# Kernel tuning notes

Hardware: AMD Instinct MI355X
Metric: run time of the kernel (lower is better)

Reference implementation:

```python
import jax, jax.numpy as jnp
import numpy as np

EPS = 1e-12  # torch F.normalize clamp epsilon
NOISE = np.array([1e-05, 2e-05, 3e-05], dtype=np.float32)  # diagonal regularizer


def setup_inputs() -> dict:
    key = jax.random.key(0)
    B, C = 65536, 128
    v_feat = jax.random.normal(key, (B, C, 3), dtype=jnp.float32)
    return {"v_feat": v_feat}


def reference(v_feat):
    # L2 normalize each 3-vector (B, C, 3) along last dim
    norm = jnp.sqrt(jnp.sum(v_feat * v_feat, axis=-1, keepdims=True))
    v = v_feat / jnp.maximum(norm, EPS)

    # Covariance M = v^T v  -> (B, 3, 3), plus tiny diagonal noise for stability
    M = jnp.einsum('bci,bcj->bij', v, v) + jnp.diag(jnp.asarray(NOISE))[None, :, :]

    # Batched symmetric 3x3 eigendecomposition (ascending eigenvalues)
    _, evecs = jnp.linalg.eigh(M)  # evecs: (B, 3, 3), columns are eigenvectors
    v1 = evecs[:, :, 0]  # (B, 3)
    v2 = evecs[:, :, 1]

    # Sign disambiguation: align with the mean direction of the features
    def fix_sign(vec):
        s = jnp.sign(jnp.sum(v * vec[:, None, :], axis=(1, 2)))  # (B,)
        s = jnp.where(s == 0, 1.0, s)
        return vec * s[:, None]

    v1 = fix_sign(v1)
    v2 = fix_sign(v2)
    v3 = jnp.cross(v1, v2)

    # Frame: columns [v1 v2 v3] -> (B, 3, 3)
    return jnp.stack([v1, v2, v3], axis=-1)
```

## Files before the change

kernel.cpp:

```cpp
#include <hip/hip_runtime.h>
#include <math.h>


#define WAVES_PER_BLOCK 4
#define BLOCK (WAVES_PER_BLOCK * 64)
#define ITERS 2
#define BATCHES_PER_WAVE (4 * ITERS)
#define BPB (WAVES_PER_BLOCK * BATCHES_PER_WAVE)

__device__ __forceinline__ double fast_rsqrt1(double x) {
    double r = (double)__builtin_amdgcn_rsqf((float)x);
    double h = -0.5 * x;
    r = r * fma(h, r * r, 1.5);
    return r;
}
__device__ __forceinline__ double fast_rsqrt2(double x) {
    double r = (double)__builtin_amdgcn_rsqf((float)x);
    double h = -0.5 * x;
    r = r * fma(h, r * r, 1.5);
    r = r * fma(h, r * r, 1.5);
    return r;
}
__device__ __forceinline__ double fast_rcp(double x) {
    double r = (double)__builtin_amdgcn_rcpf((float)x);
    r = r * fma(-x, r, 2.0);
    r = r * fma(-x, r, 2.0);
    return r;
}

template <int P, int Q, int R>
__device__ __forceinline__ void jrot(double (&A)[3][3], double (&V)[3][3]) {
    double apq = A[P][Q];
    if (fabs(apq) > 1e-18) {
        double theta = (A[Q][Q] - A[P][P]) * 0.5 * fast_rcp(apq);
        double q = fma(theta, theta, 1.0);
        double sq = (q < 1e37) ? q * fast_rsqrt2(q) : fabs(theta);
        double t = fast_rcp(fabs(theta) + sq);
        if (theta < 0.0) t = -t;
        double c = fast_rsqrt2(fma(t, t, 1.0));
        double s = t * c;
        double apq_t = t * apq;
        A[P][P] = A[P][P] - apq_t;
        A[Q][Q] = A[Q][Q] + apq_t;
        A[P][Q] = 0.0;
        A[Q][P] = 0.0;
        double apr = A[P][R], aqr = A[Q][R];
        A[P][R] = c * apr - s * aqr; A[R][P] = A[P][R];
        A[Q][R] = s * apr + c * aqr; A[R][Q] = A[Q][R];
#pragma unroll
        for (int i = 0; i < 3; ++i) {
            double vip = V[i][P], viq = V[i][Q];
            V[i][P] = c * vip - s * viq;
            V[i][Q] = s * vip + c * viq;
        }
    }
}

__global__ __launch_bounds__(BLOCK) void vn_frame_kernel(
    const float* __restrict__ vf, float* __restrict__ out, int B) {
    __shared__ double sM[BPB][9];

    const int tid  = threadIdx.x;
    const int wave = tid >> 6;
    const int lane = tid & 63;
    const int g    = lane >> 4;
    const int sub  = lane & 15;

    const int blockBase = blockIdx.x * BPB;

#pragma unroll
    for (int it = 0; it < ITERS; ++it) {
        const int bslot = wave * BATCHES_PER_WAVE + it * 4 + g;
        const int b = blockBase + bslot;
        if (b < B) {
            const float4* p4 =
                reinterpret_cast<const float4*>(vf + (size_t)b * 384 + sub * 24);
            float f[24];
#pragma unroll
            for (int i = 0; i < 6; ++i) {
                float4 q = p4[i];
                f[4 * i + 0] = q.x; f[4 * i + 1] = q.y;
                f[4 * i + 2] = q.z; f[4 * i + 3] = q.w;
            }

            double m[9];
#pragma unroll
            for (int k = 0; k < 9; ++k) m[k] = 0.0;

#pragma unroll
            for (int k = 0; k < 8; ++k) {
                float fx = f[3 * k + 0];
                float fy = f[3 * k + 1];
                float fz = f[3 * k + 2];
                float n2f = fmaf(fx, fx, fmaf(fy, fy, fz * fz));
                double n2 = (double)n2f;
                double inv = (n2 > 1e-24) ? fast_rsqrt1(n2) : 1e12;
                double x = (double)fx * inv;
                double y = (double)fy * inv;
                double z = (double)fz * inv;
                m[0] = fma(x, x, m[0]);
                m[1] = fma(x, y, m[1]);
                m[2] = fma(x, z, m[2]);
                m[3] = fma(y, y, m[3]);
                m[4] = fma(y, z, m[4]);
                m[5] = fma(z, z, m[5]);
                m[6] += x; m[7] += y; m[8] += z;
            }
#pragma unroll
            for (int off = 1; off < 16; off <<= 1) {
#pragma unroll
                for (int k = 0; k < 9; ++k) m[k] += __shfl_xor(m[k], off);
            }
            if (sub == 0) {
#pragma unroll
                for (int k = 0; k < 9; ++k) sM[bslot][k] = m[k];
            }
        }
    }

    __syncthreads();

    if (tid < BPB) {
        const int b = blockBase + tid;
        if (b < B) {
            double m[9];
#pragma unroll
            for (int k = 0; k < 9; ++k) m[k] = sM[tid][k];

            double A[3][3], V[3][3];
            A[0][0] = m[0] + (double)1e-05f;
            A[0][1] = m[1]; A[1][0] = m[1];
            A[0][2] = m[2]; A[2][0] = m[2];
            A[1][1] = m[3] + (double)2e-05f;
            A[1][2] = m[4]; A[2][1] = m[4];
            A[2][2] = m[5] + (double)3e-05f;
#pragma unroll
            for (int i = 0; i < 3; ++i)
#pragma unroll
                for (int j = 0; j < 3; ++j) V[i][j] = (i == j) ? 1.0 : 0.0;

#pragma unroll
            for (int sweep = 0; sweep < 6; ++sweep) {
                jrot<0, 1, 2>(A, V);
                jrot<0, 2, 1>(A, V);
                jrot<1, 2, 0>(A, V);
            }

            double e0 = A[0][0], e1 = A[1][1], e2 = A[2][2];
            double c0x = V[0][0], c0y = V[1][0], c0z = V[2][0];
            double c1x = V[0][1], c1y = V[1][1], c1z = V[2][1];
            double c2x = V[0][2], c2y = V[1][2], c2z = V[2][2];

#define CSWAP(ea, eb, ax, ay, az, bx, by, bz)                         \
            if (ea > eb) {                                            \
                double t_;                                            \
                t_ = ea; ea = eb; eb = t_;                            \
                t_ = ax; ax = bx; bx = t_;                            \
                t_ = ay; ay = by; by = t_;                            \
                t_ = az; az = bz; bz = t_;                            \
            }
            CSWAP(e0, e1, c0x, c0y, c0z, c1x, c1y, c1z)
            CSWAP(e1, e2, c1x, c1y, c1z, c2x, c2y, c2z)
            CSWAP(e0, e1, c0x, c0y, c0z, c1x, c1y, c1z)
#undef CSWAP

            double s0 = m[6], s1 = m[7], s2 = m[8];
            double d1 = s0 * c0x + s1 * c0y + s2 * c0z;
            double f1 = (d1 < 0.0) ? -1.0 : 1.0;
            c0x *= f1; c0y *= f1; c0z *= f1;
            double d2 = s0 * c1x + s1 * c1y + s2 * c1z;
            double f2 = (d2 < 0.0) ? -1.0 : 1.0;
            c1x *= f2; c1y *= f2; c1z *= f2;

            double v3x = c0y * c1z - c0z * c1y;
            double v3y = c0z * c1x - c0x * c1z;
            double v3z = c0x * c1y - c0y * c1x;

            float* o = out + (size_t)b * 9;
            o[0] = (float)c0x; o[1] = (float)c1x; o[2] = (float)v3x;
            o[3] = (float)c0y; o[4] = (float)c1y; o[5] = (float)v3y;
            o[6] = (float)c0z; o[7] = (float)c1z; o[8] = (float)v3z;
        }
    }
}

extern "C" void kernel_launch(void* const* d_in, const int* in_sizes, int n_in,
                              void* d_out, int out_size, void* d_ws, size_t ws_size,
                              hipStream_t stream) {
    const float* vf = (const float*)d_in[0];
    float* out = (float*)d_out;
    const int B = in_sizes[0] / 384;
    const int grid = (B + BPB - 1) / BPB;
    vn_frame_kernel<<<dim3(grid), dim3(BLOCK), 0, stream>>>(vf, out, B);
}
```

Before: 28.02 us.

## Split into reduction and eigensolve kernels with async global-to-LDS staging

The fused kernel becomes two launches. The first stages input through LDS using the async global_load_lds path with an XOR swizzle, computes the per-batch 3x3 moments, and writes them to workspace in structure-of-arrays form. The second runs the Jacobi eigensolve with one thread per batch across all lanes, where before only 32 of 256 threads did that work after a barrier. This is meant to remove idle lanes in the serial eigensolve and improve load coalescing, at the cost of a second launch and a workspace round trip.

```diff
diff --git a/kernel.cpp b/kernel.cpp
--- a/kernel.cpp
+++ b/kernel.cpp
@@ -1,12 +1,13 @@
 #include <hip/hip_runtime.h>
 #include <math.h>
-
-
-#define WAVES_PER_BLOCK 4
-#define BLOCK (WAVES_PER_BLOCK * 64)
-#define ITERS 2
-#define BATCHES_PER_WAVE (4 * ITERS)
-#define BPB (WAVES_PER_BLOCK * BATCHES_PER_WAVE)
+#include <stdint.h>
+
+
+#define BPB    16
+#define BLOCK  256
+#define NSTAGE 6
+
+__device__ __forceinline__ uint32_t swz(uint32_t q) { return q ^ ((q >> 3) & 7u); }
 
 __device__ __forceinline__ double fast_rsqrt1(double x) {
     double r = (double)__builtin_amdgcn_rsqf((float)x);
@@ -26,6 +27,81 @@
     r = r * fma(-x, r, 2.0);
     r = r * fma(-x, r, 2.0);
     return r;
+}
+
+__global__ __launch_bounds__(BLOCK) void vn_phase1(
+    const float* __restrict__ vf, double* __restrict__ wsd, int B) {
+    __shared__ float sbuf[BPB * 384];
+
+    const int tid  = threadIdx.x;
+    const int wave = tid >> 6;
+    const int lane = tid & 63;
+    const uint32_t lswz = (uint32_t)lane ^ ((uint32_t)lane >> 3);
+
+    const size_t blockQuadBase = (size_t)blockIdx.x * (BPB * 96);
+    const size_t maxQuad = (size_t)B * 96;
+
+#pragma unroll
+    for (int t = 0; t < NSTAGE; ++t) {
+        const uint32_t rowQuad = (uint32_t)(t * 4 + wave) * 64;
+        size_t gq = blockQuadBase + rowQuad + lswz;
+        if (gq >= maxQuad) gq = maxQuad - 1;
+        const float* gsrc = vf + gq * 4;
+        float* ldst = &sbuf[((size_t)rowQuad + (uint32_t)lane) * 4];
+        __builtin_amdgcn_global_load_lds(
+            (__attribute__((address_space(1))) void*)(void*)const_cast<float*>(gsrc),
+            (__attribute__((address_space(3))) void*)(void*)ldst,
+            16, 0, 0);
+    }
+    __syncthreads();
+
+    const int g    = lane >> 4;
+    const int sub  = lane & 15;
+    const int bslot = wave * 4 + g;
+    const int b = blockIdx.x * BPB + bslot;
+
+    const uint32_t baseQuad = (uint32_t)bslot * 96 + (uint32_t)sub * 6;
+    float f[24];
+#pragma unroll
+    for (int j = 0; j < 6; ++j) {
+        const uint32_t pq = swz(baseQuad + (uint32_t)j);
+        const float4 q = *reinterpret_cast<const float4*>(&sbuf[pq * 4]);
+        f[4 * j + 0] = q.x; f[4 * j + 1] = q.y;
+        f[4 * j + 2] = q.z; f[4 * j + 3] = q.w;
+    }
+
+    double m[9];
+#pragma unroll
+    for (int k = 0; k < 9; ++k) m[k] = 0.0;
+
+#pragma unroll
+    for (int k = 0; k < 8; ++k) {
+        float fx = f[3 * k + 0];
+        float fy = f[3 * k + 1];
+        float fz = f[3 * k + 2];
+        float n2f = fmaf(fx, fx, fmaf(fy, fy, fz * fz));
+        double n2 = (double)n2f;
+        double inv = (n2 > 1e-24) ? fast_rsqrt1(n2) : 1e12;
+        double x = (double)fx * inv;
+        double y = (double)fy * inv;
+        double z = (double)fz * inv;
+        m[0] = fma(x, x, m[0]);
+        m[1] = fma(x, y, m[1]);
+        m[2] = fma(x, z, m[2]);
+        m[3] = fma(y, y, m[3]);
+        m[4] = fma(y, z, m[4]);
+        m[5] = fma(z, z, m[5]);
+        m[6] += x; m[7] += y; m[8] += z;
+    }
+#pragma unroll
+    for (int off = 1; off < 16; off <<= 1) {
+#pragma unroll
+        for (int k = 0; k < 9; ++k) m[k] += __shfl_xor(m[k], off);
+    }
+    if (sub == 0 && b < B) {
+#pragma unroll
+        for (int k = 0; k < 9; ++k) wsd[(size_t)k * B + b] = m[k];
+    }
 }
 
 template <int P, int Q, int R>
@@ -56,132 +132,68 @@
     }
 }
 
-__global__ __launch_bounds__(BLOCK) void vn_frame_kernel(
-    const float* __restrict__ vf, float* __restrict__ out, int B) {
-    __shared__ double sM[BPB][9];
-
-    const int tid  = threadIdx.x;
-    const int wave = tid >> 6;
-    const int lane = tid & 63;
-    const int g    = lane >> 4;
-    const int sub  = lane & 15;
-
-    const int blockBase = blockIdx.x * BPB;
-
-#pragma unroll
-    for (int it = 0; it < ITERS; ++it) {
-        const int bslot = wave * BATCHES_PER_WAVE + it * 4 + g;
-        const int b = blockBase + bslot;
-        if (b < B) {
-            const float4* p4 =
-                reinterpret_cast<const float4*>(vf + (size_t)b * 384 + sub * 24);
-            float f[24];
-#pragma unroll
-            for (int i = 0; i < 6; ++i) {
-                float4 q = p4[i];
-                f[4 * i + 0] = q.x; f[4 * i + 1] = q.y;
-                f[4 * i + 2] = q.z; f[4 * i + 3] = q.w;
-            }
-
-            double m[9];
-#pragma unroll
-            for (int k = 0; k < 9; ++k) m[k] = 0.0;
-
-#pragma unroll
-            for (int k = 0; k < 8; ++k) {
-                float fx = f[3 * k + 0];
-                float fy = f[3 * k + 1];
-                float fz = f[3 * k + 2];
-                float n2f = fmaf(fx, fx, fmaf(fy, fy, fz * fz));
-                double n2 = (double)n2f;
-                double inv = (n2 > 1e-24) ? fast_rsqrt1(n2) : 1e12;
-                double x = (double)fx * inv;
-                double y = (double)fy * inv;
-                double z = (double)fz * inv;
-                m[0] = fma(x, x, m[0]);
-                m[1] = fma(x, y, m[1]);
-                m[2] = fma(x, z, m[2]);
-                m[3] = fma(y, y, m[3]);
-                m[4] = fma(y, z, m[4]);
-                m[5] = fma(z, z, m[5]);
-                m[6] += x; m[7] += y; m[8] += z;
-            }
-#pragma unroll
-            for (int off = 1; off < 16; off <<= 1) {
-#pragma unroll
-                for (int k = 0; k < 9; ++k) m[k] += __shfl_xor(m[k], off);
-            }
-            if (sub == 0) {
-#pragma unroll
-                for (int k = 0; k < 9; ++k) sM[bslot][k] = m[k];
-            }
-        }
-    }
-
-    __syncthreads();
-
-    if (tid < BPB) {
-        const int b = blockBase + tid;
-        if (b < B) {
-            double m[9];
-#pragma unroll
-            for (int k = 0; k < 9; ++k) m[k] = sM[tid][k];
-
-            double A[3][3], V[3][3];
-            A[0][0] = m[0] + (double)1e-05f;
-            A[0][1] = m[1]; A[1][0] = m[1];
-            A[0][2] = m[2]; A[2][0] = m[2];
-            A[1][1] = m[3] + (double)2e-05f;
-            A[1][2] = m[4]; A[2][1] = m[4];
-            A[2][2] = m[5] + (double)3e-05f;
-#pragma unroll
-            for (int i = 0; i < 3; ++i)
-#pragma unroll
-                for (int j = 0; j < 3; ++j) V[i][j] = (i == j) ? 1.0 : 0.0;
-
-#pragma unroll
-            for (int sweep = 0; sweep < 6; ++sweep) {
-                jrot<0, 1, 2>(A, V);
-                jrot<0, 2, 1>(A, V);
-                jrot<1, 2, 0>(A, V);
-            }
-
-            double e0 = A[0][0], e1 = A[1][1], e2 = A[2][2];
-            double c0x = V[0][0], c0y = V[1][0], c0z = V[2][0];
-            double c1x = V[0][1], c1y = V[1][1], c1z = V[2][1];
-            double c2x = V[0][2], c2y = V[1][2], c2z = V[2][2];
+__global__ __launch_bounds__(256) void vn_phase2(
+    const double* __restrict__ wsd, float* __restrict__ out, int B) {
+    const int b = blockIdx.x * 256 + threadIdx.x;
+    if (b >= B) return;
+
+    double m[9];
+#pragma unroll
+    for (int k = 0; k < 9; ++k) m[k] = wsd[(size_t)k * B + b];
+
+    double A[3][3], V[3][3];
+    A[0][0] = m[0] + (double)1e-05f;
+    A[0][1] = m[1]; A[1][0] = m[1];
+    A[0][2] = m[2]; A[2][0] = m[2];
+    A[1][1] = m[3] + (double)2e-05f;
+    A[1][2] = m[4]; A[2][1] = m[4];
+    A[2][2] = m[5] + (double)3e-05f;
+#pragma unroll
+    for (int i = 0; i < 3; ++i)
+#pragma unroll
+        for (int j = 0; j < 3; ++j) V[i][j] = (i == j) ? 1.0 : 0.0;
+
+#pragma unroll
+    for (int sweep = 0; sweep < 6; ++sweep) {
+        jrot<0, 1, 2>(A, V);
+        jrot<0, 2, 1>(A, V);
+        jrot<1, 2, 0>(A, V);
+    }
+
+    double e0 = A[0][0], e1 = A[1][1], e2 = A[2][2];
+    double c0x = V[0][0], c0y = V[1][0], c0z = V[2][0];
+    double c1x = V[0][1], c1y = V[1][1], c1z = V[2][1];
+    double c2x = V[0][2], c2y = V[1][2], c2z = V[2][2];
 
 #define CSWAP(ea, eb, ax, ay, az, bx, by, bz)                         \
-            if (ea > eb) {                                            \
-                double t_;                                            \
-                t_ = ea; ea = eb; eb = t_;                            \
-                t_ = ax; ax = bx; bx = t_;                            \
-                t_ = ay; ay = by; by = t_;                            \
-                t_ = az; az = bz; bz = t_;                            \
-            }
-            CSWAP(e0, e1, c0x, c0y, c0z, c1x, c1y, c1z)
-            CSWAP(e1, e2, c1x, c1y, c1z, c2x, c2y, c2z)
-            CSWAP(e0, e1, c0x, c0y, c0z, c1x, c1y, c1z)
+    if (ea > eb) {                                                    \
+        double t_;                                                    \
+        t_ = ea; ea = eb; eb = t_;                                    \
+        t_ = ax; ax = bx; bx = t_;                                    \
+        t_ = ay; ay = by; by = t_;                                    \
+        t_ = az; az = bz; bz = t_;                                    \
+    }
+    CSWAP(e0, e1, c0x, c0y, c0z, c1x, c1y, c1z)
+    CSWAP(e1, e2, c1x, c1y, c1z, c2x, c2y, c2z)
+    CSWAP(e0, e1, c0x, c0y, c0z, c1x, c1y, c1z)
 #undef CSWAP
 
-            double s0 = m[6], s1 = m[7], s2 = m[8];
-            double d1 = s0 * c0x + s1 * c0y + s2 * c0z;
-            double f1 = (d1 < 0.0) ? -1.0 : 1.0;
-            c0x *= f1; c0y *= f1; c0z *= f1;
-            double d2 = s0 * c1x + s1 * c1y + s2 * c1z;
-            double f2 = (d2 < 0.0) ? -1.0 : 1.0;
-            c1x *= f2; c1y *= f2; c1z *= f2;
-
-            double v3x = c0y * c1z - c0z * c1y;
-            double v3y = c0z * c1x - c0x * c1z;
-            double v3z = c0x * c1y - c0y * c1x;
-
-            float* o = out + (size_t)b * 9;
-            o[0] = (float)c0x; o[1] = (float)c1x; o[2] = (float)v3x;
-            o[3] = (float)c0y; o[4] = (float)c1y; o[5] = (float)v3y;
-            o[6] = (float)c0z; o[7] = (float)c1z; o[8] = (float)v3z;
-        }
-    }
+    double s0 = m[6], s1 = m[7], s2 = m[8];
+    double d1 = s0 * c0x + s1 * c0y + s2 * c0z;
+    double f1 = (d1 < 0.0) ? -1.0 : 1.0;
+    c0x *= f1; c0y *= f1; c0z *= f1;
+    double d2 = s0 * c1x + s1 * c1y + s2 * c1z;
+    double f2 = (d2 < 0.0) ? -1.0 : 1.0;
+    c1x *= f2; c1y *= f2; c1z *= f2;
+
+    double v3x = c0y * c1z - c0z * c1y;
+    double v3y = c0z * c1x - c0x * c1z;
+    double v3z = c0x * c1y - c0y * c1x;
+
+    float* o = out + (size_t)b * 9;
+    o[0] = (float)c0x; o[1] = (float)c1x; o[2] = (float)v3x;
+    o[3] = (float)c0y; o[4] = (float)c1y; o[5] = (float)v3y;
+    o[6] = (float)c0z; o[7] = (float)c1z; o[8] = (float)v3z;
 }
 
 extern "C" void kernel_launch(void* const* d_in, const int* in_sizes, int n_in,
@@ -189,7 +201,10 @@
                               hipStream_t stream) {
     const float* vf = (const float*)d_in[0];
     float* out = (float*)d_out;
+    double* wsd = (double*)d_ws;
     const int B = in_sizes[0] / 384;
-    const int grid = (B + BPB - 1) / BPB;
-    vn_frame_kernel<<<dim3(grid), dim3(BLOCK), 0, stream>>>(vf, out, B);
-}
+    const int grid1 = (B + BPB - 1) / BPB;
+    vn_phase1<<<dim3(grid1), dim3(BLOCK), 0, stream>>>(vf, wsd, B);
+    const int grid2 = (B + 255) / 256;
+    vn_phase2<<<dim3(grid2), dim3(256), 0, stream>>>(wsd, out, B);
+}
```

Result: slower. 29.62 us (+5.7%).

## Double-buffer input tiles into LDS via async global_load_lds with swizzle

Applied to the files above, without the earlier changes.

Input loading switches from direct per-thread float4 global loads to asynchronous global-to-LDS copies (global_load_lds). Each block processes four tiles of 16 batches with double buffering, and a swizzle is applied on both the copy and the read side to avoid bank conflicts. The cross-lane reduction uses DPP row_ror moves instead of shfl_xor, and the launch bounds request 3 blocks per CU. The aim is to overlap memory latency with compute and cut reduction cost, at the price of more LDS use and a __syncthreads per tile. Whether the DPP rotation and the swizzle mapping are correct depends on subtle lane semantics.

```diff
diff --git a/kernel.cpp b/kernel.cpp
--- a/kernel.cpp
+++ b/kernel.cpp
@@ -1,12 +1,16 @@
 #include <hip/hip_runtime.h>
 #include <math.h>
-
-
-#define WAVES_PER_BLOCK 4
-#define BLOCK (WAVES_PER_BLOCK * 64)
-#define ITERS 2
-#define BATCHES_PER_WAVE (4 * ITERS)
-#define BPB (WAVES_PER_BLOCK * BATCHES_PER_WAVE)
+#include <stdint.h>
+
+
+#define BLOCK      256
+#define TILE_B     16
+#define TILE_QUADS (TILE_B * 96)
+#define NT         4
+#define BPB        (TILE_B * NT)
+#define NSTAGE     6
+
+__device__ __forceinline__ uint32_t swz(uint32_t q) { return q ^ ((q >> 3) & 7u); }
 
 __device__ __forceinline__ double fast_rsqrt1(double x) {
     double r = (double)__builtin_amdgcn_rsqf((float)x);
@@ -26,6 +30,15 @@
     r = r * fma(-x, r, 2.0);
     r = r * fma(-x, r, 2.0);
     return r;
+}
+
+template <int CTRL>
+__device__ __forceinline__ double ror16_f64(double v) {
+    union { double d; int i[2]; } u, r;
+    u.d = v;
+    r.i[0] = __builtin_amdgcn_mov_dpp(u.i[0], CTRL, 0xF, 0xF, true);
+    r.i[1] = __builtin_amdgcn_mov_dpp(u.i[1], CTRL, 0xF, 0xF, true);
+    return r.d;
 }
 
 template <int P, int Q, int R>
@@ -56,76 +69,102 @@
     }
 }
 
-__global__ __launch_bounds__(BLOCK) void vn_frame_kernel(
+__global__ __launch_bounds__(BLOCK, 3) void vn_fused(
     const float* __restrict__ vf, float* __restrict__ out, int B) {
-    __shared__ double sM[BPB][9];
+    __shared__ float  sbuf[2][TILE_QUADS * 4];
+    __shared__ double sA[BPB][9];
 
     const int tid  = threadIdx.x;
     const int wave = tid >> 6;
     const int lane = tid & 63;
-    const int g    = lane >> 4;
-    const int sub  = lane & 15;
-
-    const int blockBase = blockIdx.x * BPB;
-
-#pragma unroll
-    for (int it = 0; it < ITERS; ++it) {
-        const int bslot = wave * BATCHES_PER_WAVE + it * 4 + g;
-        const int b = blockBase + bslot;
-        if (b < B) {
-            const float4* p4 =
-                reinterpret_cast<const float4*>(vf + (size_t)b * 384 + sub * 24);
-            float f[24];
-#pragma unroll
-            for (int i = 0; i < 6; ++i) {
-                float4 q = p4[i];
-                f[4 * i + 0] = q.x; f[4 * i + 1] = q.y;
-                f[4 * i + 2] = q.z; f[4 * i + 3] = q.w;
-            }
-
-            double m[9];
-#pragma unroll
-            for (int k = 0; k < 9; ++k) m[k] = 0.0;
-
-#pragma unroll
-            for (int k = 0; k < 8; ++k) {
-                float fx = f[3 * k + 0];
-                float fy = f[3 * k + 1];
-                float fz = f[3 * k + 2];
-                float n2f = fmaf(fx, fx, fmaf(fy, fy, fz * fz));
-                double n2 = (double)n2f;
-                double inv = (n2 > 1e-24) ? fast_rsqrt1(n2) : 1e12;
-                double x = (double)fx * inv;
-                double y = (double)fy * inv;
-                double z = (double)fz * inv;
-                m[0] = fma(x, x, m[0]);
-                m[1] = fma(x, y, m[1]);
-                m[2] = fma(x, z, m[2]);
-                m[3] = fma(y, y, m[3]);
-                m[4] = fma(y, z, m[4]);
-                m[5] = fma(z, z, m[5]);
-                m[6] += x; m[7] += y; m[8] += z;
-            }
-#pragma unroll
-            for (int off = 1; off < 16; off <<= 1) {
-#pragma unroll
-                for (int k = 0; k < 9; ++k) m[k] += __shfl_xor(m[k], off);
-            }
-            if (sub == 0) {
-#pragma unroll
-                for (int k = 0; k < 9; ++k) sM[bslot][k] = m[k];
-            }
-        }
+    const uint32_t lswz = (uint32_t)lane ^ ((uint32_t)lane >> 3);
+
+    const size_t maxQuad = (size_t)B * 96;
+    const size_t tile0   = (size_t)blockIdx.x * NT;
+
+    auto stage = [&](int bufi, int t) {
+#pragma unroll
+        for (int i = 0; i < NSTAGE; ++i) {
+            const uint32_t rowQuad = (uint32_t)(i * 4 + wave) * 64;
+            size_t gq = (tile0 + (size_t)t) * TILE_QUADS + rowQuad + lswz;
+            if (gq >= maxQuad) gq = maxQuad - 1;
+            const float* gsrc = vf + gq * 4;
+            float* ldst = &sbuf[bufi][((size_t)rowQuad + (uint32_t)lane) * 4];
+            __builtin_amdgcn_global_load_lds(
+                (__attribute__((address_space(1))) void*)(void*)const_cast<float*>(gsrc),
+                (__attribute__((address_space(3))) void*)(void*)ldst,
+                16, 0, 0);
+        }
+    };
+
+    stage(0, 0);
+    __syncthreads();
+
+    const int g   = lane >> 4;
+    const int sub = lane & 15;
+    const int slotInTile = wave * 4 + g;
+
+    for (int t = 0; t < NT; ++t) {
+        if (t + 1 < NT) stage((t + 1) & 1, t + 1);
+        const float* buf = sbuf[t & 1];
+
+        const uint32_t baseQuad = (uint32_t)slotInTile * 96 + (uint32_t)sub * 6;
+        float f[24];
+#pragma unroll
+        for (int j = 0; j < 6; ++j) {
+            const uint32_t pq = swz(baseQuad + (uint32_t)j);
+            const float4 q = *reinterpret_cast<const float4*>(&buf[pq * 4]);
+            f[4 * j + 0] = q.x; f[4 * j + 1] = q.y;
+            f[4 * j + 2] = q.z; f[4 * j + 3] = q.w;
+        }
+
+        double m[9];
+#pragma unroll
+        for (int k = 0; k < 9; ++k) m[k] = 0.0;
+
+#pragma unroll
+        for (int k = 0; k < 8; ++k) {
+            float fx = f[3 * k + 0];
+            float fy = f[3 * k + 1];
+            float fz = f[3 * k + 2];
+            float n2f = fmaf(fx, fx, fmaf(fy, fy, fz * fz));
+            double n2 = (double)n2f;
+            double inv = (n2 > 1e-24) ? fast_rsqrt1(n2) : 1e12;
+            double x = (double)fx * inv;
+            double y = (double)fy * inv;
+            double z = (double)fz * inv;
+            m[0] = fma(x, x, m[0]);
+            m[1] = fma(x, y, m[1]);
+            m[2] = fma(x, z, m[2]);
+            m[3] = fma(y, y, m[3]);
+            m[4] = fma(y, z, m[4]);
+            m[5] = fma(z, z, m[5]);
+            m[6] += x; m[7] += y; m[8] += z;
+        }
+
+#pragma unroll
+        for (int k = 0; k < 9; ++k) m[k] += ror16_f64<0x121>(m[k]);
+#pragma unroll
+        for (int k = 0; k < 9; ++k) m[k] += ror16_f64<0x122>(m[k]);
+#pragma unroll
+        for (int k = 0; k < 9; ++k) m[k] += ror16_f64<0x124>(m[k]);
+#pragma unroll
+        for (int k = 0; k < 9; ++k) m[k] += ror16_f64<0x128>(m[k]);
+
+        if (sub == 0) {
+            const int slot = t * TILE_B + slotInTile;
+#pragma unroll
+            for (int k = 0; k < 9; ++k) sA[slot][k] = m[k];
+        }
+        __syncthreads();
     }
 
-    __syncthreads();
-
     if (tid < BPB) {
-        const int b = blockBase + tid;
+        const int b = blockIdx.x * BPB + tid;
         if (b < B) {
             double m[9];
 #pragma unroll
-            for (int k = 0; k < 9; ++k) m[k] = sM[tid][k];
+            for (int k = 0; k < 9; ++k) m[k] = sA[tid][k];
 
             double A[3][3], V[3][3];
             A[0][0] = m[0] + (double)1e-05f;
@@ -191,5 +230,5 @@
     float* out = (float*)d_out;
     const int B = in_sizes[0] / 384;
     const int grid = (B + BPB - 1) / BPB;
-    vn_frame_kernel<<<dim3(grid), dim3(BLOCK), 0, stream>>>(vf, out, B);
-}
+    vn_fused<<<dim3(grid), dim3(BLOCK), 0, stream>>>(vf, out, B);
+}
```

After: 30.89 us. +10.2%, slower.
